# Optimization experiments

Measured on AMD Instinct MI355X. Metric: run time of the kernel, lower is better.

## Reference

```python
import jax, jax.numpy as jnp
import numpy as np

N_NODES = 50000
N_EDGES = 800000
IN_CH = 128
HID = 128


def setup_inputs() -> dict:
    key = jax.random.key(0)
    ks = jax.random.split(key, 16)
    inp = {
        "x": jax.random.normal(ks[0], (N_NODES, IN_CH), dtype=jnp.float32),
        "edge_index": jax.random.randint(ks[1], (2, N_EDGES), 0, N_NODES, dtype=jnp.int64),
        "batch_size": 1024,
    }
    dims = [(IN_CH, HID), (HID, HID), (HID, HID)]
    for i, (din, dout) in enumerate(dims):
        s = 1.0 / np.sqrt(din)
        inp[f"W_l{i}"] = jax.random.uniform(ks[2 + 4 * i], (dout, din), jnp.float32, -s, s)
        inp[f"b_l{i}"] = jax.random.uniform(ks[3 + 4 * i], (dout,), jnp.float32, -s, s)
        inp[f"W_r{i}"] = jax.random.uniform(ks[4 + 4 * i], (dout, din), jnp.float32, -s, s)
        inp[f"a{i}"] = jnp.full((dout,), 0.25, dtype=jnp.float32)  # PReLU slope
    return inp


def _sage_prelu(x, src, dst, W_l, b_l, W_r, a):
    # mean aggregation of source messages at target nodes
    msg_sum = jax.ops.segment_sum(x[src], dst, num_segments=N_NODES)  # [N, din]
    deg = jax.ops.segment_sum(jnp.ones((src.shape[0],), x.dtype), dst, num_segments=N_NODES)
    agg = msg_sum / jnp.maximum(deg, 1.0)[:, None]
    out = agg @ W_l.T + b_l + x @ W_r.T  # lin_l(aggr) + lin_r(x), bias on lin_l only
    return jnp.where(out > 0, out, a * out)  # per-channel PReLU


def reference(x, edge_index, batch_size, W_l0, b_l0, W_r0, a0, W_l1, b_l1, W_r1, a1, W_l2, b_l2, W_r2, a2):
    src, dst = edge_index[0], edge_index[1]
    x = _sage_prelu(x, src, dst, W_l0, b_l0, W_r0, a0)
    x = _sage_prelu(x, src, dst, W_l1, b_l1, W_r1, a1)
    x = _sage_prelu(x, src, dst, W_l2, b_l2, W_r2, a2)
    return x[:batch_size]
```

## Files before the change

kernel.cpp:

```cpp
#include <hip/hip_runtime.h>

#define NN 50000
#define NE 800000
#define C 128
#define SCAN_BLOCKS ((NN + 255) / 256)
#define ASTRIDE 136

typedef __attribute__((ext_vector_type(8))) short bf16x8;
typedef __attribute__((ext_vector_type(4))) float f32x4;
typedef unsigned short ushort;

__device__ inline ushort bf16_rn(float f) {
    unsigned u = __builtin_bit_cast(unsigned, f);
    u += 0x7FFF + ((u >> 16) & 1);
    return (ushort)(u >> 16);
}
__device__ inline void split_bf16(float f, ushort& hi, ushort& lo) {
    hi = bf16_rn(f);
    float hif = __builtin_bit_cast(float, (unsigned)hi << 16);
    lo = bf16_rn(f - hif);
}


__global__ __launch_bounds__(256)
void count_pos_kernel(const int* __restrict__ dst, int* __restrict__ deg,
                      int* __restrict__ pos, int n_edges) {
    int e0 = (blockIdx.x * blockDim.x + threadIdx.x) * 4;
    if (e0 >= n_edges) return;
    int4 d4 = *(const int4*)(dst + e0);
    int p0 = atomicAdd(&deg[d4.x], 1);
    int p1 = atomicAdd(&deg[d4.y], 1);
    int p2 = atomicAdd(&deg[d4.z], 1);
    int p3 = atomicAdd(&deg[d4.w], 1);
    *(int4*)(pos + e0) = make_int4(p0, p1, p2, p3);
}

__global__ __launch_bounds__(256)
void scan1_kernel(const int* __restrict__ deg, int* __restrict__ row_ptr,
                  float* __restrict__ inv_deg, int* __restrict__ bsum, int n) {
    __shared__ int wsum[4];
    __shared__ int wpre[4];
    int t = threadIdx.x, lane = t & 63, w = t >> 6;
    int i = blockIdx.x * 256 + t;
    int v = (i < n) ? deg[i] : 0;
    int s = v;
    #pragma unroll
    for (int off = 1; off < 64; off <<= 1) {
        int y = __shfl_up(s, off, 64);
        if (lane >= off) s += y;
    }
    if (lane == 63) wsum[w] = s;
    __syncthreads();
    if (t == 0) {
        int acc = 0;
        #pragma unroll
        for (int j = 0; j < 4; ++j) { wpre[j] = acc; acc += wsum[j]; }
        bsum[blockIdx.x] = acc;
    }
    __syncthreads();
    if (i < n) {
        row_ptr[i] = wpre[w] + (s - v);
        inv_deg[i] = 1.0f / (float)max(v, 1);
    }
}

__global__ __launch_bounds__(256)
void scan2_kernel(const int* __restrict__ bsum, int* __restrict__ boff,
                  int* __restrict__ row_ptr, int nb, int n) {
    __shared__ int wsum[4];
    __shared__ int wpre[4];
    int t = threadIdx.x, lane = t & 63, w = t >> 6;
    int v = (t < nb) ? bsum[t] : 0;
    int s = v;
    #pragma unroll
    for (int off = 1; off < 64; off <<= 1) {
        int y = __shfl_up(s, off, 64);
        if (lane >= off) s += y;
    }
    if (lane == 63) wsum[w] = s;
    __syncthreads();
    if (t == 0) {
        int acc = 0;
        #pragma unroll
        for (int j = 0; j < 4; ++j) { wpre[j] = acc; acc += wsum[j]; }
        row_ptr[n] = acc;
    }
    __syncthreads();
    if (t < nb) boff[t] = wpre[w] + (s - v);
}

__global__ __launch_bounds__(256)
void scan3_kernel(int* __restrict__ row_ptr, const int* __restrict__ boff, int n) {
    int i = blockIdx.x * 256 + threadIdx.x;
    if (i < n) row_ptr[i] += boff[blockIdx.x];
}


__global__ __launch_bounds__(256)
void fill2_kernel(const int* __restrict__ src, const int* __restrict__ dst,
                  const int* __restrict__ row_ptr, const int* __restrict__ pos,
                  int* __restrict__ col, int n_edges) {
    int e0 = (blockIdx.x * blockDim.x + threadIdx.x) * 4;
    if (e0 >= n_edges) return;
    int4 d4 = *(const int4*)(dst + e0);
    int4 s4 = *(const int4*)(src + e0);
    int4 p4 = *(const int4*)(pos + e0);
    col[row_ptr[d4.x] + p4.x] = s4.x;
    col[row_ptr[d4.y] + p4.y] = s4.y;
    col[row_ptr[d4.z] + p4.z] = s4.z;
    col[row_ptr[d4.w] + p4.w] = s4.w;
}


__global__ __launch_bounds__(256)
void split_kernel(const float* __restrict__ in, ushort* __restrict__ h,
                  ushort* __restrict__ l, int n4) {
    int i = blockIdx.x * 256 + threadIdx.x;
    if (i >= n4) return;
    f32x4 v = ((const f32x4*)in)[i];
    ushort h0, h1, h2, h3, l0, l1, l2, l3;
    split_bf16(v.x, h0, l0);
    split_bf16(v.y, h1, l1);
    split_bf16(v.z, h2, l2);
    split_bf16(v.w, h3, l3);
    *(uint2*)(h + i * 4) = make_uint2((unsigned)h0 | ((unsigned)h1 << 16),
                                      (unsigned)h2 | ((unsigned)h3 << 16));
    *(uint2*)(l + i * 4) = make_uint2((unsigned)l0 | ((unsigned)l1 << 16),
                                      (unsigned)l2 | ((unsigned)l3 << 16));
}


__global__ __launch_bounds__(256)
void agg_kernel(const ushort* __restrict__ xh, const int* __restrict__ row_ptr,
                const int* __restrict__ col, const float* __restrict__ inv_deg,
                float* __restrict__ agg, int nodes) {
    int node = (blockIdx.x * blockDim.x + threadIdx.x) >> 6;
    int lane = threadIdx.x & 63;
    if (node >= nodes) return;
    int start = row_ptr[node], end = row_ptr[node + 1];
    const unsigned* xr = (const unsigned*)xh;
    float ax = 0.f, ay = 0.f;
    int e = start;
    for (; e + 7 < end; e += 8) {
        unsigned u[8];
        #pragma unroll
        for (int j = 0; j < 8; ++j) u[j] = xr[(size_t)col[e + j] * 64 + lane];
        #pragma unroll
        for (int j = 0; j < 8; ++j) {
            ax += __builtin_bit_cast(float, u[j] << 16);
            ay += __builtin_bit_cast(float, u[j] & 0xFFFF0000u);
        }
    }
    for (; e + 1 < end; e += 2) {
        unsigned u0 = xr[(size_t)col[e] * 64 + lane];
        unsigned u1 = xr[(size_t)col[e + 1] * 64 + lane];
        ax += __builtin_bit_cast(float, u0 << 16) + __builtin_bit_cast(float, u1 << 16);
        ay += __builtin_bit_cast(float, u0 & 0xFFFF0000u) + __builtin_bit_cast(float, u1 & 0xFFFF0000u);
    }
    if (e < end) {
        unsigned u = xr[(size_t)col[e] * 64 + lane];
        ax += __builtin_bit_cast(float, u << 16);
        ay += __builtin_bit_cast(float, u & 0xFFFF0000u);
    }
    float inv = inv_deg[node];
    *(float2*)(agg + (size_t)node * C + lane * 2) = make_float2(ax * inv, ay * inv);
}


__global__ __launch_bounds__(256, 3)
void gemm_kernel(const float* __restrict__ Ain,
                 const ushort* __restrict__ Xh, const ushort* __restrict__ Xl,
                 const float* __restrict__ Wl, const float* __restrict__ bl,
                 const float* __restrict__ Wr, const float* __restrict__ slope,
                 float* __restrict__ outf, ushort* __restrict__ outh,
                 ushort* __restrict__ outl, int rows) {
    __shared__ ushort Ahi[64 * ASTRIDE];
    __shared__ ushort Alo[64 * ASTRIDE];
    int t = threadIdx.x;
    int lane = t & 63;
    int w = t >> 6;
    int l = lane & 15;
    int q = lane >> 4;
    int row0 = blockIdx.x * 64;

    f32x4 acc[4][2];
    #pragma unroll
    for (int mt = 0; mt < 4; ++mt)
        #pragma unroll
        for (int nt = 0; nt < 2; ++nt)
            acc[mt][nt] = (f32x4){0.f, 0.f, 0.f, 0.f};

    #pragma unroll
    for (int mat = 0; mat < 2; ++mat) {
        const float* W = mat ? Wr : Wl;

        bf16x8 bhi[2][4], blo[2][4];
        #pragma unroll
        for (int nt = 0; nt < 2; ++nt) {
            int n = w * 32 + nt * 16 + l;
            const float* wp = W + n * C + q * 8;
            #pragma unroll
            for (int kb = 0; kb < 4; ++kb) {
                f32x4 w0 = *(const f32x4*)(wp + kb * 32);
                f32x4 w1 = *(const f32x4*)(wp + kb * 32 + 4);
                float f[8] = {w0.x, w0.y, w0.z, w0.w, w1.x, w1.y, w1.z, w1.w};
                bf16x8 h, o;
                #pragma unroll
                for (int j = 0; j < 8; ++j) {
                    ushort hh, ll;
                    split_bf16(f[j], hh, ll);
                    h[j] = (short)hh;
                    o[j] = (short)ll;
                }
                bhi[nt][kb] = h;
                blo[nt][kb] = o;
            }
        }

        __syncthreads();
        int ar = t >> 2;
        int aq = t & 3;
        int r = min(row0 + ar, rows - 1);
        ushort* dh = Ahi + ar * ASTRIDE + aq * 32;
        ushort* dl = Alo + ar * ASTRIDE + aq * 32;
        if (mat == 0) {
            const float* ap = Ain + (size_t)r * C + aq * 32;
            #pragma unroll
            for (int i = 0; i < 8; ++i) {
                f32x4 v = *(const f32x4*)(ap + i * 4);
                ushort h0, h1, h2, h3, l0, l1, l2, l3;
                split_bf16(v.x, h0, l0);
                split_bf16(v.y, h1, l1);
                split_bf16(v.z, h2, l2);
                split_bf16(v.w, h3, l3);
                *(uint2*)(dh + i * 4) = make_uint2((unsigned)h0 | ((unsigned)h1 << 16),
                                                   (unsigned)h2 | ((unsigned)h3 << 16));
                *(uint2*)(dl + i * 4) = make_uint2((unsigned)l0 | ((unsigned)l1 << 16),
                                                   (unsigned)l2 | ((unsigned)l3 << 16));
            }
        } else {
            const ushort* ph = Xh + (size_t)r * C + aq * 32;
            const ushort* pl = Xl + (size_t)r * C + aq * 32;
            #pragma unroll
            for (int i = 0; i < 4; ++i) {
                *(uint4*)(dh + i * 8) = *(const uint4*)(ph + i * 8);
                *(uint4*)(dl + i * 8) = *(const uint4*)(pl + i * 8);
            }
        }
        __syncthreads();

        #pragma unroll
        for (int kb = 0; kb < 4; ++kb) {
            #pragma unroll
            for (int mt = 0; mt < 4; ++mt) {
                int off = (mt * 16 + l) * ASTRIDE + kb * 32 + q * 8;
                bf16x8 ahi = *(const bf16x8*)(Ahi + off);
                bf16x8 alo = *(const bf16x8*)(Alo + off);
                #pragma unroll
                for (int nt = 0; nt < 2; ++nt) {
                    acc[mt][nt] = __builtin_amdgcn_mfma_f32_16x16x32_bf16(ahi, bhi[nt][kb], acc[mt][nt], 0, 0, 0);
                    acc[mt][nt] = __builtin_amdgcn_mfma_f32_16x16x32_bf16(alo, bhi[nt][kb], acc[mt][nt], 0, 0, 0);
                    acc[mt][nt] = __builtin_amdgcn_mfma_f32_16x16x32_bf16(ahi, blo[nt][kb], acc[mt][nt], 0, 0, 0);
                }
            }
        }
    }

    #pragma unroll
    for (int nt = 0; nt < 2; ++nt) {
        int n = w * 32 + nt * 16 + l;
        float b = bl[n], s = slope[n];
        #pragma unroll
        for (int mt = 0; mt < 4; ++mt) {
            #pragma unroll
            for (int rg = 0; rg < 4; ++rg) {
                int r = row0 + mt * 16 + q * 4 + rg;
                if (r < rows) {
                    float v = acc[mt][nt][rg] + b;
                    v = v > 0.f ? v : s * v;
                    if (outf) {
                        outf[(size_t)r * C + n] = v;
                    } else {
                        ushort hh, ll;
                        split_bf16(v, hh, ll);
                        outh[(size_t)r * C + n] = hh;
                        outl[(size_t)r * C + n] = ll;
                    }
                }
            }
        }
    }
}


extern "C" void kernel_launch(void* const* d_in, const int* in_sizes, int n_in,
                              void* d_out, int out_size, void* d_ws, size_t ws_size,
                              hipStream_t stream) {
    const float* x   = (const float*)d_in[0];
    const int*   src = (const int*)d_in[1];
    const int*   dst = src + NE;
    const float* Wl[3] = {(const float*)d_in[3], (const float*)d_in[7],  (const float*)d_in[11]};
    const float* bl[3] = {(const float*)d_in[4], (const float*)d_in[8],  (const float*)d_in[12]};
    const float* Wr[3] = {(const float*)d_in[5], (const float*)d_in[9],  (const float*)d_in[13]};
    const float* sl[3] = {(const float*)d_in[6], (const float*)d_in[10], (const float*)d_in[14]};

    int*   deg     = (int*)d_ws;
    int*   row_ptr = deg + 50016;
    int*   col     = row_ptr + 50016;
    int*   pos     = col + 800000;
    float* inv_deg = (float*)(pos + 800000);
    int*   bsum    = (int*)(inv_deg + 50016);
    int*   boff    = bsum + 256;
    float* agg     = (float*)(boff + 256);
    ushort* Ah     = (ushort*)(agg + (size_t)NN * C);
    ushort* Al     = Ah + (size_t)NN * C;
    ushort* Bh     = Al + (size_t)NN * C;
    ushort* Bl     = Bh + (size_t)NN * C;

    hipMemsetAsync(deg, 0, 50016 * sizeof(int), stream);

    const int E4B = (NE / 4 + 255) / 256;
    count_pos_kernel<<<E4B, 256, 0, stream>>>(dst, deg, pos, NE);
    scan1_kernel<<<SCAN_BLOCKS, 256, 0, stream>>>(deg, row_ptr, inv_deg, bsum, NN);
    scan2_kernel<<<1, 256, 0, stream>>>(bsum, boff, row_ptr, SCAN_BLOCKS, NN);
    scan3_kernel<<<SCAN_BLOCKS, 256, 0, stream>>>(row_ptr, boff, NN);
    fill2_kernel<<<E4B, 256, 0, stream>>>(src, dst, row_ptr, pos, col, NE);

    split_kernel<<<(NN * C / 4 + 255) / 256, 256, 0, stream>>>(x, Ah, Al, NN * C / 4);

    int rows_out = out_size / C;

    agg_kernel<<<(NN + 3) / 4, 256, 0, stream>>>(Ah, row_ptr, col, inv_deg, agg, NN);
    gemm_kernel<<<(NN + 63) / 64, 256, 0, stream>>>(agg, Ah, Al, Wl[0], bl[0], Wr[0], sl[0],
                                                    nullptr, Bh, Bl, NN);

    agg_kernel<<<(NN + 3) / 4, 256, 0, stream>>>(Bh, row_ptr, col, inv_deg, agg, NN);
    gemm_kernel<<<(NN + 63) / 64, 256, 0, stream>>>(agg, Bh, Bl, Wl[1], bl[1], Wr[1], sl[1],
                                                    nullptr, Ah, Al, NN);

    agg_kernel<<<(rows_out + 3) / 4, 256, 0, stream>>>(Ah, row_ptr, col, inv_deg, agg, rows_out);
    gemm_kernel<<<(rows_out + 63) / 64, 256, 0, stream>>>(agg, Ah, Al, Wl[2], bl[2], Wr[2], sl[2],
                                                          (float*)d_out, nullptr, nullptr, rows_out);
}
```

Baseline: 319.6 us.

## Fuse neighbor mean aggregation into the per-layer GEMM kernel

The separate aggregation kernel is removed. Each GEMM block now gathers the neighbor bf16 rows for its 64 nodes itself, takes the mean, splits the result into hi/lo bf16 and writes it straight into shared memory. This drops the fp32 agg buffer write and re-read in every layer, and the inv_deg array is replaced by computing the degree from row_ptr. The cost is that the latency-bound gather now runs under the GEMM's launch bounds (3 blocks per CU), with each wave walking 16 rows in sequence. The edge-counting and CSR-fill kernels also each handle 8 edges per thread instead of 4.

```diff
diff --git a/kernel.cpp b/kernel.cpp
--- a/kernel.cpp
+++ b/kernel.cpp
@@ -25,19 +25,25 @@
 __global__ __launch_bounds__(256)
 void count_pos_kernel(const int* __restrict__ dst, int* __restrict__ deg,
                       int* __restrict__ pos, int n_edges) {
-    int e0 = (blockIdx.x * blockDim.x + threadIdx.x) * 4;
+    int e0 = (blockIdx.x * 256 + threadIdx.x) * 8;
     if (e0 >= n_edges) return;
-    int4 d4 = *(const int4*)(dst + e0);
-    int p0 = atomicAdd(&deg[d4.x], 1);
-    int p1 = atomicAdd(&deg[d4.y], 1);
-    int p2 = atomicAdd(&deg[d4.z], 1);
-    int p3 = atomicAdd(&deg[d4.w], 1);
-    *(int4*)(pos + e0) = make_int4(p0, p1, p2, p3);
+    int4 a = *(const int4*)(dst + e0);
+    int4 b = *(const int4*)(dst + e0 + 4);
+    int p0 = atomicAdd(&deg[a.x], 1);
+    int p1 = atomicAdd(&deg[a.y], 1);
+    int p2 = atomicAdd(&deg[a.z], 1);
+    int p3 = atomicAdd(&deg[a.w], 1);
+    int p4 = atomicAdd(&deg[b.x], 1);
+    int p5 = atomicAdd(&deg[b.y], 1);
+    int p6 = atomicAdd(&deg[b.z], 1);
+    int p7 = atomicAdd(&deg[b.w], 1);
+    *(int4*)(pos + e0)     = make_int4(p0, p1, p2, p3);
+    *(int4*)(pos + e0 + 4) = make_int4(p4, p5, p6, p7);
 }
 
 __global__ __launch_bounds__(256)
 void scan1_kernel(const int* __restrict__ deg, int* __restrict__ row_ptr,
-                  float* __restrict__ inv_deg, int* __restrict__ bsum, int n) {
+                  int* __restrict__ bsum, int n) {
     __shared__ int wsum[4];
     __shared__ int wpre[4];
     int t = threadIdx.x, lane = t & 63, w = t >> 6;
@@ -58,10 +64,7 @@
         bsum[blockIdx.x] = acc;
     }
     __syncthreads();
-    if (i < n) {
-        row_ptr[i] = wpre[w] + (s - v);
-        inv_deg[i] = 1.0f / (float)max(v, 1);
-    }
+    if (i < n) row_ptr[i] = wpre[w] + (s - v);
 }
 
 __global__ __launch_bounds__(256)
@@ -100,15 +103,22 @@
 void fill2_kernel(const int* __restrict__ src, const int* __restrict__ dst,
                   const int* __restrict__ row_ptr, const int* __restrict__ pos,
                   int* __restrict__ col, int n_edges) {
-    int e0 = (blockIdx.x * blockDim.x + threadIdx.x) * 4;
+    int e0 = (blockIdx.x * 256 + threadIdx.x) * 8;
     if (e0 >= n_edges) return;
-    int4 d4 = *(const int4*)(dst + e0);
-    int4 s4 = *(const int4*)(src + e0);
-    int4 p4 = *(const int4*)(pos + e0);
-    col[row_ptr[d4.x] + p4.x] = s4.x;
-    col[row_ptr[d4.y] + p4.y] = s4.y;
-    col[row_ptr[d4.z] + p4.z] = s4.z;
-    col[row_ptr[d4.w] + p4.w] = s4.w;
+    int4 da = *(const int4*)(dst + e0);
+    int4 db = *(const int4*)(dst + e0 + 4);
+    int4 sa = *(const int4*)(src + e0);
+    int4 sb = *(const int4*)(src + e0 + 4);
+    int4 pa = *(const int4*)(pos + e0);
+    int4 pb = *(const int4*)(pos + e0 + 4);
+    col[row_ptr[da.x] + pa.x] = sa.x;
+    col[row_ptr[da.y] + pa.y] = sa.y;
+    col[row_ptr[da.z] + pa.z] = sa.z;
+    col[row_ptr[da.w] + pa.w] = sa.w;
+    col[row_ptr[db.x] + pb.x] = sb.x;
+    col[row_ptr[db.y] + pb.y] = sb.y;
+    col[row_ptr[db.z] + pb.z] = sb.z;
+    col[row_ptr[db.w] + pb.w] = sb.w;
 }
 
 
@@ -130,50 +140,13 @@
 }
 
 
-__global__ __launch_bounds__(256)
-void agg_kernel(const ushort* __restrict__ xh, const int* __restrict__ row_ptr,
-                const int* __restrict__ col, const float* __restrict__ inv_deg,
-                float* __restrict__ agg, int nodes) {
-    int node = (blockIdx.x * blockDim.x + threadIdx.x) >> 6;
-    int lane = threadIdx.x & 63;
-    if (node >= nodes) return;
-    int start = row_ptr[node], end = row_ptr[node + 1];
-    const unsigned* xr = (const unsigned*)xh;
-    float ax = 0.f, ay = 0.f;
-    int e = start;
-    for (; e + 7 < end; e += 8) {
-        unsigned u[8];
-        #pragma unroll
-        for (int j = 0; j < 8; ++j) u[j] = xr[(size_t)col[e + j] * 64 + lane];
-        #pragma unroll
-        for (int j = 0; j < 8; ++j) {
-            ax += __builtin_bit_cast(float, u[j] << 16);
-            ay += __builtin_bit_cast(float, u[j] & 0xFFFF0000u);
-        }
-    }
-    for (; e + 1 < end; e += 2) {
-        unsigned u0 = xr[(size_t)col[e] * 64 + lane];
-        unsigned u1 = xr[(size_t)col[e + 1] * 64 + lane];
-        ax += __builtin_bit_cast(float, u0 << 16) + __builtin_bit_cast(float, u1 << 16);
-        ay += __builtin_bit_cast(float, u0 & 0xFFFF0000u) + __builtin_bit_cast(float, u1 & 0xFFFF0000u);
-    }
-    if (e < end) {
-        unsigned u = xr[(size_t)col[e] * 64 + lane];
-        ax += __builtin_bit_cast(float, u << 16);
-        ay += __builtin_bit_cast(float, u & 0xFFFF0000u);
-    }
-    float inv = inv_deg[node];
-    *(float2*)(agg + (size_t)node * C + lane * 2) = make_float2(ax * inv, ay * inv);
-}
-
-
 __global__ __launch_bounds__(256, 3)
-void gemm_kernel(const float* __restrict__ Ain,
-                 const ushort* __restrict__ Xh, const ushort* __restrict__ Xl,
-                 const float* __restrict__ Wl, const float* __restrict__ bl,
-                 const float* __restrict__ Wr, const float* __restrict__ slope,
-                 float* __restrict__ outf, ushort* __restrict__ outh,
-                 ushort* __restrict__ outl, int rows) {
+void layer_kernel(const ushort* __restrict__ Xh, const ushort* __restrict__ Xl,
+                  const int* __restrict__ row_ptr, const int* __restrict__ col,
+                  const float* __restrict__ Wl, const float* __restrict__ bl,
+                  const float* __restrict__ Wr, const float* __restrict__ slope,
+                  float* __restrict__ outf, ushort* __restrict__ outh,
+                  ushort* __restrict__ outl, int rows) {
     __shared__ ushort Ahi[64 * ASTRIDE];
     __shared__ ushort Alo[64 * ASTRIDE];
     int t = threadIdx.x;
@@ -217,28 +190,53 @@
             }
         }
 
-        __syncthreads();
-        int ar = t >> 2;
-        int aq = t & 3;
-        int r = min(row0 + ar, rows - 1);
-        ushort* dh = Ahi + ar * ASTRIDE + aq * 32;
-        ushort* dl = Alo + ar * ASTRIDE + aq * 32;
         if (mat == 0) {
-            const float* ap = Ain + (size_t)r * C + aq * 32;
-            #pragma unroll
-            for (int i = 0; i < 8; ++i) {
-                f32x4 v = *(const f32x4*)(ap + i * 4);
-                ushort h0, h1, h2, h3, l0, l1, l2, l3;
-                split_bf16(v.x, h0, l0);
-                split_bf16(v.y, h1, l1);
-                split_bf16(v.z, h2, l2);
-                split_bf16(v.w, h3, l3);
-                *(uint2*)(dh + i * 4) = make_uint2((unsigned)h0 | ((unsigned)h1 << 16),
-                                                   (unsigned)h2 | ((unsigned)h3 << 16));
-                *(uint2*)(dl + i * 4) = make_uint2((unsigned)l0 | ((unsigned)l1 << 16),
-                                                   (unsigned)l2 | ((unsigned)l3 << 16));
+            const unsigned* xr = (const unsigned*)Xh;
+            for (int j = 0; j < 16; ++j) {
+                int m = w * 16 + j;
+                int r = row0 + m;
+                float ax = 0.f, ay = 0.f;
+                if (r < rows) {
+                    int start = row_ptr[r], end = row_ptr[r + 1];
+                    int e = start;
+                    for (; e + 7 < end; e += 8) {
+                        unsigned u[8];
+                        #pragma unroll
+                        for (int k = 0; k < 8; ++k) u[k] = xr[(size_t)col[e + k] * 64 + lane];
+                        #pragma unroll
+                        for (int k = 0; k < 8; ++k) {
+                            ax += __builtin_bit_cast(float, u[k] << 16);
+                            ay += __builtin_bit_cast(float, u[k] & 0xFFFF0000u);
+                        }
+                    }
+                    for (; e + 1 < end; e += 2) {
+                        unsigned u0 = xr[(size_t)col[e] * 64 + lane];
+                        unsigned u1 = xr[(size_t)col[e + 1] * 64 + lane];
+                        ax += __builtin_bit_cast(float, u0 << 16) + __builtin_bit_cast(float, u1 << 16);
+                        ay += __builtin_bit_cast(float, u0 & 0xFFFF0000u) + __builtin_bit_cast(float, u1 & 0xFFFF0000u);
+                    }
+                    if (e < end) {
+                        unsigned u = xr[(size_t)col[e] * 64 + lane];
+                        ax += __builtin_bit_cast(float, u << 16);
+                        ay += __builtin_bit_cast(float, u & 0xFFFF0000u);
+                    }
+                    float inv = 1.0f / (float)max(end - start, 1);
+                    ax *= inv;
+                    ay *= inv;
+                }
+                ushort ha, la, hb, lb;
+                split_bf16(ax, ha, la);
+                split_bf16(ay, hb, lb);
+                *(unsigned*)(Ahi + m * ASTRIDE + lane * 2) = (unsigned)ha | ((unsigned)hb << 16);
+                *(unsigned*)(Alo + m * ASTRIDE + lane * 2) = (unsigned)la | ((unsigned)lb << 16);
             }
         } else {
+            __syncthreads();
+            int ar = t >> 2;
+            int aq = t & 3;
+            int r = min(row0 + ar, rows - 1);
+            ushort* dh = Ahi + ar * ASTRIDE + aq * 32;
+            ushort* dl = Alo + ar * ASTRIDE + aq * 32;
             const ushort* ph = Xh + (size_t)r * C + aq * 32;
             const ushort* pl = Xl + (size_t)r * C + aq * 32;
             #pragma unroll
@@ -308,37 +306,33 @@
     int*   row_ptr = deg + 50016;
     int*   col     = row_ptr + 50016;
     int*   pos     = col + 800000;
-    float* inv_deg = (float*)(pos + 800000);
-    int*   bsum    = (int*)(inv_deg + 50016);
+    int*   bsum    = pos + 800000;
     int*   boff    = bsum + 256;
-    float* agg     = (float*)(boff + 256);
-    ushort* Ah     = (ushort*)(agg + (size_t)NN * C);
+    ushort* Ah     = (ushort*)(boff + 256);
     ushort* Al     = Ah + (size_t)NN * C;
     ushort* Bh     = Al + (size_t)NN * C;
     ushort* Bl     = Bh + (size_t)NN * C;
 
     hipMemsetAsync(deg, 0, 50016 * sizeof(int), stream);
 
-    const int E4B = (NE / 4 + 255) / 256;
-    count_pos_kernel<<<E4B, 256, 0, stream>>>(dst, deg, pos, NE);
-    scan1_kernel<<<SCAN_BLOCKS, 256, 0, stream>>>(deg, row_ptr, inv_deg, bsum, NN);
+    const int E8B = (NE / 8 + 255) / 256;
+    count_pos_kernel<<<E8B, 256, 0, stream>>>(dst, deg, pos, NE);
+    scan1_kernel<<<SCAN_BLOCKS, 256, 0, stream>>>(deg, row_ptr, bsum, NN);
     scan2_kernel<<<1, 256, 0, stream>>>(bsum, boff, row_ptr, SCAN_BLOCKS, NN);
     scan3_kernel<<<SCAN_BLOCKS, 256, 0, stream>>>(row_ptr, boff, NN);
-    fill2_kernel<<<E4B, 256, 0, stream>>>(src, dst, row_ptr, pos, col, NE);
+    fill2_kernel<<<E8B, 256, 0, stream>>>(src, dst, row_ptr, pos, col, NE);
 
     split_kernel<<<(NN * C / 4 + 255) / 256, 256, 0, stream>>>(x, Ah, Al, NN * C / 4);
 
     int rows_out = out_size / C;
 
-    agg_kernel<<<(NN + 3) / 4, 256, 0, stream>>>(Ah, row_ptr, col, inv_deg, agg, NN);
-    gemm_kernel<<<(NN + 63) / 64, 256, 0, stream>>>(agg, Ah, Al, Wl[0], bl[0], Wr[0], sl[0],
-                                                    nullptr, Bh, Bl, NN);
-
-    agg_kernel<<<(NN + 3) / 4, 256, 0, stream>>>(Bh, row_ptr, col, inv_deg, agg, NN);
-    gemm_kernel<<<(NN + 63) / 64, 256, 0, stream>>>(agg, Bh, Bl, Wl[1], bl[1], Wr[1], sl[1],
-                                                    nullptr, Ah, Al, NN);
-
-    agg_kernel<<<(rows_out + 3) / 4, 256, 0, stream>>>(Ah, row_ptr, col, inv_deg, agg, rows_out);
-    gemm_kernel<<<(rows_out + 63) / 64, 256, 0, stream>>>(agg, Ah, Al, Wl[2], bl[2], Wr[2], sl[2],
-                                                          (float*)d_out, nullptr, nullptr, rows_out);
-}
+    layer_kernel<<<(NN + 63) / 64, 256, 0, stream>>>(Ah, Al, row_ptr, col,
+                                                     Wl[0], bl[0], Wr[0], sl[0],
+                                                     nullptr, Bh, Bl, NN);
+    layer_kernel<<<(NN + 63) / 64, 256, 0, stream>>>(Bh, Bl, row_ptr, col,
+                                                     Wl[1], bl[1], Wr[1], sl[1],
+                                                     nullptr, Ah, Al, NN);
+    layer_kernel<<<(rows_out + 63) / 64, 256, 0, stream>>>(Ah, Al, row_ptr, col,
+                                                           Wl[2], bl[2], Wr[2], sl[2],
+                                                           (float*)d_out, nullptr, nullptr, rows_out);
+}
```

New measurement: 449.4 us. 40.6% more time.
